# Kernel tuning notes

Measured on AMD Instinct MI355X. Metric: run time of the kernel, lower is better.

The kernel has to match this reference:

```python
import jax, jax.numpy as jnp
import numpy as np
import math

SQRT5 = math.sqrt(5.0)


def setup_inputs() -> dict:
    key = jax.random.key(0)
    k1, k2, k3, k4 = jax.random.split(key, 4)
    N1, N2, D = 8192, 8192, 64
    X1 = jax.random.normal(k1, (N1, D), dtype=jnp.float32)
    X2 = jax.random.normal(k2, (N2, D), dtype=jnp.float32)
    # positive scaling / lengthscale, kept away from 0 for numerical sanity
    c = jax.random.uniform(k3, (1,), dtype=jnp.float32) + 0.5
    l = jax.random.uniform(k4, (D,), dtype=jnp.float32) + 0.5
    return {"X1": X1, "X2": X2, "c": c, "l": l}


def _matern52(X1, X2, c, l):
    X1_l = X1 / l  # [N1, D]
    X2_l = X2 / l  # [N2, D]
    # pairwise Euclidean distance via the expansion ||a-b||^2 = ||a||^2 + ||b||^2 - 2 a.b
    # (avoids materializing the [N1, N2, D] broadcasted difference tensor)
    sq1 = jnp.sum(X1_l * X1_l, axis=-1)  # [N1]
    sq2 = jnp.sum(X2_l * X2_l, axis=-1)  # [N2]
    cross = jnp.einsum("nd,md->nm", X1_l, X2_l)  # [N1, N2]
    d2 = jnp.maximum(sq1[:, None] + sq2[None, :] - 2.0 * cross, 0.0)
    r = jnp.sqrt(d2)  # [N1, N2]
    c2 = jnp.squeeze(c * c)
    return c2 * (1.0 + SQRT5 * r + (5.0 / 3.0) * (r * r)) * jnp.exp(-SQRT5 * r)


def reference(X1, X2, c, l):
    return _matern52(X1, X2, c, l)
```

## Files before the change

### kernel.cpp

```cpp
#include <hip/hip_runtime.h>
#include <math.h>

#define N_DIM 64
#define TILE  128

typedef unsigned short ushort_t;
typedef unsigned int   uint_t;
typedef _Float16 f16x8 __attribute__((ext_vector_type(8)));
typedef _Float16 f16x4 __attribute__((ext_vector_type(4)));
typedef float    f32x4 __attribute__((ext_vector_type(4)));

__device__ __forceinline__ int swz16(int row, int kc) {
    return (row << 7) + ((kc ^ (row & 7)) << 4);
}

typedef __attribute__((address_space(1))) const void gas_void;
typedef __attribute__((address_space(3))) void       las_void;
__device__ __forceinline__ void gload16(const void* g, void* l) {
    __builtin_amdgcn_global_load_lds((gas_void*)g, (las_void*)l, 16, 0, 0);
}

__global__ __launch_bounds__(256)
void matern52_prep_kernel(const float* __restrict__ X1,
                          const float* __restrict__ X2,
                          const float* __restrict__ l,
                          unsigned char* __restrict__ dstA,
                          unsigned char* __restrict__ dstB,
                          float* __restrict__ sq1,
                          float* __restrict__ sq2,
                          int N1)
{
    const int t  = threadIdx.x;
    const int kq = t & 15;
    int row = blockIdx.x * 16 + (t >> 4);

    const float* __restrict__ X;
    unsigned char* __restrict__ dst;
    float* __restrict__ sq;
    if (row < N1) { X = X1; dst = dstA; sq = sq1; }
    else          { X = X2; dst = dstB; sq = sq2; row -= N1; }

    float4 lv = *reinterpret_cast<const float4*>(&l[kq * 4]);
    float4 x  = *reinterpret_cast<const float4*>(&X[(size_t)row * N_DIM + kq * 4]);
    const float a0 = x.x / lv.x, a1 = x.y / lv.y, a2 = x.z / lv.z, a3 = x.w / lv.w;

    float s = a0 * a0;
    s = fmaf(a1, a1, s); s = fmaf(a2, a2, s); s = fmaf(a3, a3, s);
    s += __shfl_xor(s, 1);
    s += __shfl_xor(s, 2);
    s += __shfl_xor(s, 4);
    s += __shfl_xor(s, 8);
    if (kq == 0) sq[row] = s;

    f16x4 h = { (_Float16)a0, (_Float16)a1, (_Float16)a2, (_Float16)a3 };
    const int off = (row << 7) + ((((kq >> 1) ^ (row & 7))) << 4) + ((kq & 1) << 3);
    *reinterpret_cast<f16x4*>(dst + off) = h;
}

__global__ __launch_bounds__(256, 4)
void matern52_main_kernel(const unsigned char* __restrict__ A16,
                          const unsigned char* __restrict__ B16,
                          const float* __restrict__ sq1,
                          const float* __restrict__ sq2,
                          const float* __restrict__ cc,
                          float* __restrict__ out,
                          int N1, int N2, int nbx, int chunk)
{
    __shared__ __align__(16) unsigned char lds[2 * TILE * N_DIM * 2];

    const int t = threadIdx.x;

    const int orig  = blockIdx.x;
    const int newid = (orig & 7) * chunk + (orig >> 3);
    const int bi    = newid / nbx;
    const int bj    = newid % nbx;

    unsigned char* ldsA = lds;
    unsigned char* ldsB = lds + TILE * N_DIM * 2;

    {
        const unsigned char* srcA = A16 + (size_t)bi * (TILE * 128);
        const unsigned char* srcB = B16 + (size_t)bj * (TILE * 128);
        const int wbase = (t >> 6) << 10;
        const int gb    = t * 16;
        #pragma unroll
        for (int i = 0; i < 4; ++i) {
            gload16(srcA + i * 4096 + gb, ldsA + i * 4096 + wbase);
            gload16(srcB + i * 4096 + gb, ldsB + i * 4096 + wbase);
        }
    }
    __syncthreads();

    const int wid  = t >> 6;
    const int lane = t & 63;
    const int wtr  = wid >> 1;
    const int wtc  = wid & 1;
    const int fr   = lane & 15;
    const int kg   = lane >> 4;

    f32x4 acc[4][4] = {};

    #pragma unroll
    for (int kk = 0; kk < 2; ++kk) {
        f16x8 af[4], bg[4];
        #pragma unroll
        for (int m = 0; m < 4; ++m)
            af[m] = *reinterpret_cast<const f16x8*>(
                ldsA + swz16(wtr * 64 + m * 16 + fr, kk * 4 + kg));
        #pragma unroll
        for (int n = 0; n < 4; ++n)
            bg[n] = *reinterpret_cast<const f16x8*>(
                ldsB + swz16(wtc * 64 + n * 16 + fr, kk * 4 + kg));
        #pragma unroll
        for (int m = 0; m < 4; ++m)
            #pragma unroll
            for (int n = 0; n < 4; ++n)
                acc[m][n] = __builtin_amdgcn_mfma_f32_16x16x32_f16(
                    bg[n], af[m], acc[m][n], 0, 0, 0);
    }

    __syncthreads();

    const float c0 = cc[0];
    const float SQ5   = 2.23606797749979f;
    const float FIVE3 = 1.66666666666667f;
    const float NK    = -3.22617785847899f;
    const float l2c2  = 2.885390081777927f * __logf(c0);

    const float* sqA = sq1 + bi * TILE;
    const float* sqB = sq2 + bj * TILE + wtc * 64;

    unsigned char* scr = lds + (wid << 12);

    f32x4 sb4[4];
    #pragma unroll
    for (int n = 0; n < 4; ++n)
        sb4[n] = *reinterpret_cast<const f32x4*>(sqB + n * 16 + kg * 4);

    const int r_off = lane >> 4;
    const int c16   = lane & 15;

    #pragma unroll
    for (int m = 0; m < 4; ++m) {
        const float sa = sqA[wtr * 64 + m * 16 + fr];

        #pragma unroll
        for (int n = 0; n < 4; ++n) {
            f32x4 v = acc[m][n];
            f32x4 res;
            #pragma unroll
            for (int q = 0; q < 4; ++q) {
                float d2 = fmaxf(fmaf(-2.0f, v[q], sa + sb4[n][q]), 0.0f);
                float r  = __builtin_amdgcn_sqrtf(d2);
                float e  = __builtin_amdgcn_exp2f(fmaf(NK, r, l2c2));
                res[q] = fmaf(FIVE3, d2, fmaf(SQ5, r, 1.0f)) * e;
            }
            const int boff = (fr << 8) + ((((n << 6) + (kg << 4))) ^ ((fr & 7) << 4));
            *reinterpret_cast<f32x4*>(scr + boff) = res;
        }

        __builtin_amdgcn_wave_barrier();

        #pragma unroll
        for (int i = 0; i < 4; ++i) {
            const int rr = i * 4 + r_off;
            const int rb = (rr << 8) + ((c16 << 4) ^ ((rr & 7) << 4));
            f32x4 val = *reinterpret_cast<const f32x4*>(scr + rb);
            const int grow = wtr * 64 + m * 16 + rr;
            float* p = out + ((size_t)(bi * TILE) + grow) * (size_t)N2
                           + (size_t)(bj * TILE) + wtc * 64 + c16 * 4;
            __builtin_nontemporal_store(val, reinterpret_cast<f32x4*>(p));
        }

        __builtin_amdgcn_wave_barrier();
    }
}

__device__ __forceinline__ ushort_t f2bf(float f) {
    uint_t u = __float_as_uint(f);
    u += 0x7FFFu + ((u >> 16) & 1u);
    return (ushort_t)(u >> 16);
}
__device__ __forceinline__ float bf2f(ushort_t h) {
    return __uint_as_float(((uint_t)h) << 16);
}
typedef short s16x8 __attribute__((ext_vector_type(8)));

__global__ __launch_bounds__(512, 4)
void matern52_fallback_kernel(const float* __restrict__ X1,
                              const float* __restrict__ X2,
                              const float* __restrict__ cc,
                              const float* __restrict__ l,
                              float* __restrict__ out,
                              int N1, int N2)
{
    __shared__ ushort_t Ah[TILE * N_DIM], Al[TILE * N_DIM];
    __shared__ ushort_t Bh[TILE * N_DIM], Bl[TILE * N_DIM];
    __shared__ float sqA[TILE], sqB[TILE];

    const int t  = threadIdx.x;
    const int bi = blockIdx.y, bj = blockIdx.x;
    const int kq   = t & 15;
    const int rsub = t >> 4;

    float4 lv = *reinterpret_cast<const float4*>(&l[kq * 4]);
    const float rlx = 1.f / lv.x, rly = 1.f / lv.y, rlz = 1.f / lv.z, rlw = 1.f / lv.w;
    const float* x1b = X1 + (size_t)(bi * TILE) * N_DIM;
    const float* x2b = X2 + (size_t)(bj * TILE) * N_DIM;

    #define STAGE(Xb, Th, Tl, SQ)                                              \
    {                                                                          \
        _Pragma("unroll")                                                      \
        for (int c = 0; c < 4; ++c) {                                          \
            const int row = c * 32 + rsub;                                     \
            float4 x = *reinterpret_cast<const float4*>(&(Xb)[row * N_DIM + kq * 4]); \
            float a0 = x.x * rlx, a1 = x.y * rly, a2 = x.z * rlz, a3 = x.w * rlw; \
            ushort_t h0 = f2bf(a0), h1 = f2bf(a1), h2 = f2bf(a2), h3 = f2bf(a3); \
            ushort_t e0 = f2bf(a0 - bf2f(h0)), e1 = f2bf(a1 - bf2f(h1));       \
            ushort_t e2 = f2bf(a2 - bf2f(h2)), e3 = f2bf(a3 - bf2f(h3));       \
            const int off = (row << 7) + (((kq >> 1) << 4) ^ ((row & 7) << 4)) + ((kq & 1) << 3); \
            uint2 hv, lvv;                                                     \
            hv.x  = (uint_t)h0 | ((uint_t)h1 << 16);                           \
            hv.y  = (uint_t)h2 | ((uint_t)h3 << 16);                           \
            lvv.x = (uint_t)e0 | ((uint_t)e1 << 16);                           \
            lvv.y = (uint_t)e2 | ((uint_t)e3 << 16);                           \
            *reinterpret_cast<uint2*>((char*)(Th) + off) = hv;                 \
            *reinterpret_cast<uint2*>((char*)(Tl) + off) = lvv;                \
            float s = a0 * a0;                                                 \
            s = fmaf(a1, a1, s); s = fmaf(a2, a2, s); s = fmaf(a3, a3, s);     \
            s += __shfl_xor(s, 1);                                             \
            s += __shfl_xor(s, 2);                                             \
            s += __shfl_xor(s, 4);                                             \
            s += __shfl_xor(s, 8);                                             \
            if (kq == 0) (SQ)[row] = s;                                        \
        }                                                                      \
    }
    STAGE(x1b, Ah, Al, sqA)
    STAGE(x2b, Bh, Bl, sqB)
    #undef STAGE
    __syncthreads();

    const int wid  = t >> 6;
    const int lane = t & 63;
    const int wtr = wid >> 1, wtc = wid & 1;
    const int fr  = lane & 15, kg = lane >> 4;

    f32x4 acc[2][4] = {};
    #pragma unroll
    for (int pass = 0; pass < 3; ++pass) {
        const ushort_t* TA = (pass == 2) ? Al : Ah;
        const ushort_t* TB = (pass == 1) ? Bl : Bh;
        #pragma unroll
        for (int kk = 0; kk < 2; ++kk) {
            s16x8 af[2], bg[4];
            #pragma unroll
            for (int m = 0; m < 2; ++m)
                af[m] = *reinterpret_cast<const s16x8*>(
                    (const char*)TA + swz16(wtr * 32 + m * 16 + fr, kk * 4 + kg));
            #pragma unroll
            for (int n = 0; n < 4; ++n)
                bg[n] = *reinterpret_cast<const s16x8*>(
                    (const char*)TB + swz16(wtc * 64 + n * 16 + fr, kk * 4 + kg));
            #pragma unroll
            for (int m = 0; m < 2; ++m)
                #pragma unroll
                for (int n = 0; n < 4; ++n)
                    acc[m][n] = __builtin_amdgcn_mfma_f32_16x16x32_bf16(
                        bg[n], af[m], acc[m][n], 0, 0, 0);
        }
    }

    const float c0 = cc[0];
    const float SQ5   = 2.23606797749979f;
    const float FIVE3 = 1.66666666666667f;
    const float lnc2  = 2.0f * __logf(c0);

    #pragma unroll
    for (int m = 0; m < 2; ++m) {
        const int row_l = wtr * 32 + m * 16 + fr;
        const float sa = sqA[row_l];
        float* rowp = out + ((size_t)(bi * TILE) + row_l) * (size_t)N2
                          + (size_t)(bj * TILE) + wtc * 64;
        #pragma unroll
        for (int n = 0; n < 4; ++n) {
            const int cb = n * 16 + kg * 4;
            f32x4 sb4 = *reinterpret_cast<const f32x4*>(&sqB[wtc * 64 + cb]);
            f32x4 v = acc[m][n];
            f32x4 res;
            #pragma unroll
            for (int q = 0; q < 4; ++q) {
                float d2 = fmaxf(fmaf(-2.0f, v[q], sa + sb4[q]), 0.0f);
                float r  = sqrtf(d2);
                float e  = __expf(fmaf(-SQ5, r, lnc2));
                res[q] = fmaf(FIVE3, d2, fmaf(SQ5, r, 1.0f)) * e;
            }
            *reinterpret_cast<f32x4*>(rowp + cb) = res;
        }
    }
}

extern "C" void kernel_launch(void* const* d_in, const int* in_sizes, int n_in,
                              void* d_out, int out_size, void* d_ws, size_t ws_size,
                              hipStream_t stream) {
    const float* X1 = (const float*)d_in[0];
    const float* X2 = (const float*)d_in[1];
    const float* c  = (const float*)d_in[2];
    const float* l  = (const float*)d_in[3];
    float* out = (float*)d_out;

    const int N1 = in_sizes[0] / N_DIM;
    const int N2 = in_sizes[1] / N_DIM;

    const size_t aBytes = (size_t)N1 * 128;
    const size_t bBytes = (size_t)N2 * 128;
    const size_t needWs = aBytes + bBytes + (size_t)(N1 + N2) * sizeof(float);

    const int nby  = N1 / TILE;
    const int nbx  = N2 / TILE;
    const int nblk = nby * nbx;

    const bool shapeOK = (N1 % TILE == 0) && (N2 % TILE == 0) &&
                         (N1 % 16 == 0) && (nblk % 8 == 0);

    if (ws_size >= needWs && shapeOK) {
        unsigned char* A16 = (unsigned char*)d_ws;
        unsigned char* B16 = A16 + aBytes;
        float* sq1 = (float*)(B16 + bBytes);
        float* sq2 = sq1 + N1;

        matern52_prep_kernel<<<dim3((N1 + N2) / 16), 256, 0, stream>>>(
            X1, X2, l, A16, B16, sq1, sq2, N1);

        matern52_main_kernel<<<dim3(nblk), 256, 0, stream>>>(
            A16, B16, sq1, sq2, c, out, N1, N2, nbx, nblk / 8);
    } else {
        dim3 grid(N2 / TILE, N1 / TILE);
        matern52_fallback_kernel<<<grid, 512, 0, stream>>>(X1, X2, c, l, out, N1, N2);
    }
}
```

Measured before the change: 56.17 us.

## Make main kernel persistent over column tiles with prefetched B and resident A

Each block now owns a 64-row strip and walks 8 consecutive 128-column tiles, keeping its A fragments in registers. The next B tile is loaded asynchronously into LDS while the current tile's epilogue (sqrt/exp and store) runs. The output-staging scratch is moved to a separate LDS region. This cuts block count, launch and reload overhead and overlaps loads with the store-bound epilogue. In exchange, LDS per block grows, tiles get smaller, the grid shrinks and the XCD-aware block remapping is dropped.

```diff
diff --git a/kernel.cpp b/kernel.cpp
--- a/kernel.cpp
+++ b/kernel.cpp
@@ -3,6 +3,9 @@
 
 #define N_DIM 64
 #define TILE  128
+#define BMR   64
+#define BNC   128
+#define NTJ   8
 
 typedef unsigned short ushort_t;
 typedef unsigned int   uint_t;
@@ -64,30 +67,29 @@
                           const float* __restrict__ sq2,
                           const float* __restrict__ cc,
                           float* __restrict__ out,
-                          int N1, int N2, int nbx, int chunk)
+                          int N1, int N2)
 {
-    __shared__ __align__(16) unsigned char lds[2 * TILE * N_DIM * 2];
-
-    const int t = threadIdx.x;
-
-    const int orig  = blockIdx.x;
-    const int newid = (orig & 7) * chunk + (orig >> 3);
-    const int bi    = newid / nbx;
-    const int bj    = newid % nbx;
+    __shared__ __align__(16) unsigned char lds[8192 + 16384 + 16384];
+
+    const int t   = threadIdx.x;
+    const int bi  = blockIdx.y;
+    const int bj0 = blockIdx.x * NTJ;
 
     unsigned char* ldsA = lds;
-    unsigned char* ldsB = lds + TILE * N_DIM * 2;
+    unsigned char* ldsB = lds + 8192;
+
+    const int wbase = (t >> 6) << 10;
+    const int gb    = t * 16;
 
     {
-        const unsigned char* srcA = A16 + (size_t)bi * (TILE * 128);
-        const unsigned char* srcB = B16 + (size_t)bj * (TILE * 128);
-        const int wbase = (t >> 6) << 10;
-        const int gb    = t * 16;
-        #pragma unroll
-        for (int i = 0; i < 4; ++i) {
+        const unsigned char* srcA = A16 + (size_t)bi * (BMR * 128);
+        #pragma unroll
+        for (int i = 0; i < 2; ++i)
             gload16(srcA + i * 4096 + gb, ldsA + i * 4096 + wbase);
+        const unsigned char* srcB = B16 + (size_t)bj0 * (BNC * 128);
+        #pragma unroll
+        for (int i = 0; i < 4; ++i)
             gload16(srcB + i * 4096 + gb, ldsB + i * 4096 + wbase);
-        }
     }
     __syncthreads();
 
@@ -98,28 +100,13 @@
     const int fr   = lane & 15;
     const int kg   = lane >> 4;
 
-    f32x4 acc[4][4] = {};
-
+    f16x8 afr[2][2];
     #pragma unroll
-    for (int kk = 0; kk < 2; ++kk) {
-        f16x8 af[4], bg[4];
-        #pragma unroll
-        for (int m = 0; m < 4; ++m)
-            af[m] = *reinterpret_cast<const f16x8*>(
-                ldsA + swz16(wtr * 64 + m * 16 + fr, kk * 4 + kg));
-        #pragma unroll
-        for (int n = 0; n < 4; ++n)
-            bg[n] = *reinterpret_cast<const f16x8*>(
-                ldsB + swz16(wtc * 64 + n * 16 + fr, kk * 4 + kg));
-        #pragma unroll
-        for (int m = 0; m < 4; ++m)
-            #pragma unroll
-            for (int n = 0; n < 4; ++n)
-                acc[m][n] = __builtin_amdgcn_mfma_f32_16x16x32_f16(
-                    bg[n], af[m], acc[m][n], 0, 0, 0);
-    }
-
-    __syncthreads();
+    for (int kk = 0; kk < 2; ++kk)
+        #pragma unroll
+        for (int m = 0; m < 2; ++m)
+            afr[kk][m] = *reinterpret_cast<const f16x8*>(
+                ldsA + swz16(wtr * 32 + m * 16 + fr, kk * 4 + kg));
 
     const float c0 = cc[0];
     const float SQ5   = 2.23606797749979f;
@@ -127,52 +114,82 @@
     const float NK    = -3.22617785847899f;
     const float l2c2  = 2.885390081777927f * __logf(c0);
 
-    const float* sqA = sq1 + bi * TILE;
-    const float* sqB = sq2 + bj * TILE + wtc * 64;
-
-    unsigned char* scr = lds + (wid << 12);
-
-    f32x4 sb4[4];
-    #pragma unroll
-    for (int n = 0; n < 4; ++n)
-        sb4[n] = *reinterpret_cast<const f32x4*>(sqB + n * 16 + kg * 4);
-
+    const float* sqA = sq1 + bi * BMR;
+    const float sa_m[2] = { sqA[wtr * 32 + fr], sqA[wtr * 32 + 16 + fr] };
+
+    unsigned char* scr = lds + 24576 + (wid << 12);
     const int r_off = lane >> 4;
     const int c16   = lane & 15;
 
-    #pragma unroll
-    for (int m = 0; m < 4; ++m) {
-        const float sa = sqA[wtr * 64 + m * 16 + fr];
-
-        #pragma unroll
-        for (int n = 0; n < 4; ++n) {
-            f32x4 v = acc[m][n];
-            f32x4 res;
-            #pragma unroll
-            for (int q = 0; q < 4; ++q) {
-                float d2 = fmaxf(fmaf(-2.0f, v[q], sa + sb4[n][q]), 0.0f);
-                float r  = __builtin_amdgcn_sqrtf(d2);
-                float e  = __builtin_amdgcn_exp2f(fmaf(NK, r, l2c2));
-                res[q] = fmaf(FIVE3, d2, fmaf(SQ5, r, 1.0f)) * e;
+    for (int j = 0; j < NTJ; ++j) {
+        f32x4 acc[2][4] = {};
+        #pragma unroll
+        for (int kk = 0; kk < 2; ++kk) {
+            f16x8 bg[4];
+            #pragma unroll
+            for (int n = 0; n < 4; ++n)
+                bg[n] = *reinterpret_cast<const f16x8*>(
+                    ldsB + swz16(wtc * 64 + n * 16 + fr, kk * 4 + kg));
+            #pragma unroll
+            for (int m = 0; m < 2; ++m)
+                #pragma unroll
+                for (int n = 0; n < 4; ++n)
+                    acc[m][n] = __builtin_amdgcn_mfma_f32_16x16x32_f16(
+                        bg[n], afr[kk][m], acc[m][n], 0, 0, 0);
+        }
+
+        __syncthreads();
+
+        if (j < NTJ - 1) {
+            const unsigned char* srcB = B16 + (size_t)(bj0 + j + 1) * (BNC * 128);
+            #pragma unroll
+            for (int i = 0; i < 4; ++i)
+                gload16(srcB + i * 4096 + gb, ldsB + i * 4096 + wbase);
+        }
+
+        const int bj = bj0 + j;
+        const float* sqB = sq2 + bj * BNC + wtc * 64;
+        f32x4 sb4[4];
+        #pragma unroll
+        for (int n = 0; n < 4; ++n)
+            sb4[n] = *reinterpret_cast<const f32x4*>(sqB + n * 16 + kg * 4);
+
+        #pragma unroll
+        for (int m = 0; m < 2; ++m) {
+            const float sa = sa_m[m];
+
+            #pragma unroll
+            for (int n = 0; n < 4; ++n) {
+                f32x4 v = acc[m][n];
+                f32x4 res;
+                #pragma unroll
+                for (int q = 0; q < 4; ++q) {
+                    float d2 = fmaxf(fmaf(-2.0f, v[q], sa + sb4[n][q]), 0.0f);
+                    float r  = __builtin_amdgcn_sqrtf(d2);
+                    float e  = __builtin_amdgcn_exp2f(fmaf(NK, r, l2c2));
+                    res[q] = fmaf(FIVE3, d2, fmaf(SQ5, r, 1.0f)) * e;
+                }
+                const int boff = (fr << 8) + ((((n << 6) + (kg << 4))) ^ ((fr & 7) << 4));
+                *reinterpret_cast<f32x4*>(scr + boff) = res;
             }
-            const int boff = (fr << 8) + ((((n << 6) + (kg << 4))) ^ ((fr & 7) << 4));
-            *reinterpret_cast<f32x4*>(scr + boff) = res;
-        }
-
-        __builtin_amdgcn_wave_barrier();
-
-        #pragma unroll
-        for (int i = 0; i < 4; ++i) {
-            const int rr = i * 4 + r_off;
-            const int rb = (rr << 8) + ((c16 << 4) ^ ((rr & 7) << 4));
-            f32x4 val = *reinterpret_cast<const f32x4*>(scr + rb);
-            const int grow = wtr * 64 + m * 16 + rr;
-            float* p = out + ((size_t)(bi * TILE) + grow) * (size_t)N2
-                           + (size_t)(bj * TILE) + wtc * 64 + c16 * 4;
-            __builtin_nontemporal_store(val, reinterpret_cast<f32x4*>(p));
-        }
-
-        __builtin_amdgcn_wave_barrier();
+
+            __builtin_amdgcn_wave_barrier();
+
+            #pragma unroll
+            for (int i = 0; i < 4; ++i) {
+                const int rr = i * 4 + r_off;
+                const int rb = (rr << 8) + ((c16 << 4) ^ ((rr & 7) << 4));
+                f32x4 val = *reinterpret_cast<const f32x4*>(scr + rb);
+                const int grow = wtr * 32 + m * 16 + rr;
+                float* p = out + ((size_t)(bi * BMR) + grow) * (size_t)N2
+                               + (size_t)bj * BNC + wtc * 64 + c16 * 4;
+                __builtin_nontemporal_store(val, reinterpret_cast<f32x4*>(p));
+            }
+
+            __builtin_amdgcn_wave_barrier();
+        }
+
+        __syncthreads();
     }
 }
 
@@ -315,12 +332,8 @@
     const size_t bBytes = (size_t)N2 * 128;
     const size_t needWs = aBytes + bBytes + (size_t)(N1 + N2) * sizeof(float);
 
-    const int nby  = N1 / TILE;
-    const int nbx  = N2 / TILE;
-    const int nblk = nby * nbx;
-
-    const bool shapeOK = (N1 % TILE == 0) && (N2 % TILE == 0) &&
-                         (N1 % 16 == 0) && (nblk % 8 == 0);
+    const bool shapeOK = (N1 % BMR == 0) && (N2 % (BNC * NTJ) == 0) &&
+                         (N1 % 16 == 0) && (N2 % 16 == 0);
 
     if (ws_size >= needWs && shapeOK) {
         unsigned char* A16 = (unsigned char*)d_ws;
@@ -331,8 +344,9 @@
         matern52_prep_kernel<<<dim3((N1 + N2) / 16), 256, 0, stream>>>(
             X1, X2, l, A16, B16, sq1, sq2, N1);
 
-        matern52_main_kernel<<<dim3(nblk), 256, 0, stream>>>(
-            A16, B16, sq1, sq2, c, out, N1, N2, nbx, nblk / 8);
+        dim3 grid(N2 / (BNC * NTJ), N1 / BMR);
+        matern52_main_kernel<<<grid, 256, 0, stream>>>(
+            A16, B16, sq1, sq2, c, out, N1, N2);
     } else {
         dim3 grid(N2 / TILE, N1 / TILE);
         matern52_fallback_kernel<<<grid, 512, 0, stream>>>(X1, X2, c, l, out, N1, N2);
```

After: 73.46 us. 1.31x slower.
